# Performance work log

Hardware: AMD Instinct MI355X
Metric: run time of the kernel (lower is better)

The kernel has to match this reference:

```python
import jax, jax.numpy as jnp
import numpy as np
from jax import lax

C = 64
KD = 16  # in_channels // k_factor
KS = 3
DN = ('NCHW', 'OIHW', 'NCHW')


def setup_inputs() -> dict:
    key = jax.random.key(0)
    ks = jax.random.split(key, 9)
    B, H, W = 4, 128, 128
    s = 0.05
    return {
        'x': jax.random.normal(ks[0], (B, C, H, W), jnp.float32),
        'y': jax.random.normal(ks[1], (B, C, H, W), jnp.float32),
        'z': jax.random.normal(ks[2], (B, C, H, W), jnp.float32),
        'Wq': jax.random.normal(ks[3], (C, 1, KS, KS), jnp.float32) * s,   # depthwise
        'bq': jax.random.normal(ks[4], (C,), jnp.float32) * s,
        'Wk': jax.random.normal(ks[5], (KD, C, KS, KS), jnp.float32) * s,
        'bk': jax.random.normal(ks[6], (KD,), jnp.float32) * s,
        'wv': jax.random.normal(ks[7], (KD,), jnp.float32) * s,           # 1x1 conv 1->KD
        'bv': jax.random.normal(ks[8], (KD,), jnp.float32) * s,
    }


def reference(x, y, z, Wq, bq, Wk, bk, wv, bv):
    # Q: depthwise 3x3 conv + ReLU on y -> [B,C,H,W]
    q = jax.nn.relu(
        lax.conv_general_dilated(y, Wq, (1, 1), 'SAME',
                                 dimension_numbers=DN, feature_group_count=C)
        + bq[None, :, None, None])
    # K: 3x3 conv C->KD + ReLU on x -> [B,KD,H,W], shared across the C channel axis
    k = jax.nn.relu(
        lax.conv_general_dilated(x, Wk, (1, 1), 'SAME', dimension_numbers=DN)
        + bk[None, :, None, None])
    # V: 1x1 conv 1->KD + ReLU applied per input channel of z -> [B,C,KD,H,W]
    v = jax.nn.relu(z[:, :, None] * wv[None, None, :, None, None]
                    + bv[None, None, :, None, None])
    # Degenerate SDPA: head_dim=1 so scale=1; softmax over the KD 'sequence' axis.
    scores = q[:, :, None] * k[:, None]              # [B,C,KD,H,W]
    attn = jax.nn.softmax(scores, axis=2)
    return jnp.sum(attn * v, axis=2)                 # [B,C,H,W]
```

## Files before the change

kernel.cpp:

```cpp
#include <hip/hip_runtime.h>

#define HH 128
#define WW 128
#define CC 64
#define KD 16
#define HW (HH * WW)
#define HWB (HW * 4)
#define TOTBYTES (4u * CC * HW * 4u)
#define OOB_SENT 0x40000000

typedef __attribute__((ext_vector_type(4))) int   int32x4_t;
typedef __attribute__((ext_vector_type(4))) float floatx4;
typedef __attribute__((ext_vector_type(2))) float floatx2;

__device__ floatx4 llvm_amdgcn_raw_buffer_load_v4f32(int32x4_t srsrc, int voffset,
                                                     int soffset, int aux)
    __asm("llvm.amdgcn.raw.buffer.load.v4f32");
__device__ floatx2 llvm_amdgcn_raw_buffer_load_v2f32(int32x4_t srsrc, int voffset,
                                                     int soffset, int aux)
    __asm("llvm.amdgcn.raw.buffer.load.v2f32");

__device__ inline int32x4_t make_srd(const void* p, unsigned bytes) {
    const unsigned long long a = (unsigned long long)p;
    int32x4_t r;
    r.x = (int)(a & 0xffffffffull);
    r.y = (int)(a >> 32);
    r.z = (int)bytes;
    r.w = 0x00020000;
    return r;
}

#if __has_builtin(__builtin_amdgcn_exp2f)
#define FAST_EXP2(x) __builtin_amdgcn_exp2f(x)
#define KLOG2E 1.44269504088896340736f
#else
#define FAST_EXP2(x) __expf(x)
#define KLOG2E 1.0f
#endif

__global__ __launch_bounds__(512, 4) void gatev_fused(
    const float* __restrict__ x, const float* __restrict__ y,
    const float* __restrict__ z,
    const float* __restrict__ Wq, const float* __restrict__ bq,
    const float* __restrict__ Wk, const float* __restrict__ bk,
    const float* __restrict__ wv, const float* __restrict__ bv,
    float* __restrict__ out)
{
    __shared__ float lds[16384];

    const int tid  = threadIdx.x;
    const int g    = __builtin_amdgcn_readfirstlane(tid >> 6);
    const int lane = tid & 63;
    const int px16 = lane & 15, py = lane >> 4;
    const int b    = blockIdx.z;
    const int w0   = blockIdx.x * 32 + px16 * 2;
    const int h    = blockIdx.y * 4 + py;
    const int pix  = h * WW + w0;
    const int p0   = py * 32 + px16 * 2;

    const int32x4_t rx = make_srd(x, TOTBYTES);
    const int32x4_t ry = make_srd(y, TOTBYTES);
    const int32x4_t rz = make_srd(z, TOTBYTES);

    const int colb = (w0 > 0 ? w0 - 1 : 0) * 4;
    int rowB[3];
#pragma unroll
    for (int r = 0; r < 3; ++r) {
        const int rr = h - 1 + r;
        rowB[r] = (rr >= 0 && rr < HH) ? rr * WW * 4 + colb : OOB_SENT;
    }
    const float mL = (w0 > 0) ? 1.f : 0.f;
    const float mR = (w0 + 2 < WW) ? 1.f : 0.f;
    const bool  w0e = (w0 == 0);

    const int base = b * CC * HWB;
    const int c0   = __builtin_amdgcn_readfirstlane(g * 8);

    {
        const int d  = tid & 15;
        const int cA = tid >> 4;
#pragma unroll
        for (int half = 0; half < 2; ++half) {
            const int c   = cA + half * 32;
            const int dst = (c >> 3) * 1152 + (c & 7) * 144 + d;
            const float* src = Wk + (d * CC + c) * 9;
#pragma unroll
            for (int t = 0; t < 9; ++t)
                lds[dst + t * 16] = src[t];
        }
    }
    __syncthreads();

    floatx2 aP0[8], aP1[8];
#pragma unroll
    for (int i = 0; i < 8; ++i) { aP0[i] = (floatx2){0.f, 0.f}; aP1[i] = (floatx2){0.f, 0.f}; }

    auto load3 = [&](floatx4 (&f)[3], int so) {
#pragma unroll
        for (int r = 0; r < 3; ++r)
            f[r] = llvm_amdgcn_raw_buffer_load_v4f32(rx, rowB[r], so, 0);
    };
    auto mktaps = [&](const floatx4& f, float (&s)[4]) {
        s[0] = f.x * mL;
        s[1] = w0e ? f.x : f.y;
        s[2] = w0e ? f.y : f.z;
        s[3] = (w0e ? f.z : f.w) * mR;
    };
    auto compute = [&](const floatx4 (&f)[3], int wb) {
        float s[3][4];
#pragma unroll
        for (int r = 0; r < 3; ++r) mktaps(f[r], s[r]);
#pragma unroll
        for (int t = 0; t < 9; ++t) {
            const int tr = t / 3, tc = t % 3;
            const floatx2 t0 = {s[tr][tc],     s[tr][tc]};
            const floatx2 t1 = {s[tr][tc + 1], s[tr][tc + 1]};
#pragma unroll
            for (int j = 0; j < 4; ++j) {
                const floatx4 w4 = *(const floatx4*)&lds[wb + t * 16 + j * 4];
                const floatx2 lo = __builtin_shufflevector(w4, w4, 0, 1);
                const floatx2 hi = __builtin_shufflevector(w4, w4, 2, 3);
                aP0[2 * j + 0] = __builtin_elementwise_fma(lo, t0, aP0[2 * j + 0]);
                aP0[2 * j + 1] = __builtin_elementwise_fma(hi, t0, aP0[2 * j + 1]);
                aP1[2 * j + 0] = __builtin_elementwise_fma(lo, t1, aP1[2 * j + 0]);
                aP1[2 * j + 1] = __builtin_elementwise_fma(hi, t1, aP1[2 * j + 1]);
            }
        }
    };

    const int wbase = g * 1152;
    floatx4 f0[3], f1[3];
    load3(f0, base + c0 * HWB);
#pragma unroll
    for (int cp = 0; cp < 4; ++cp) {
        load3(f1, base + (c0 + 2 * cp + 1) * HWB);
        compute(f0, wbase + (2 * cp) * 144);
        load3(f0, base + (c0 + 2 * cp + 2) * HWB);
        compute(f1, wbase + (2 * cp + 1) * 144);
    }
    __syncthreads();

#pragma unroll
    for (int i = 0; i < 8; ++i) {
        *(floatx2*)&lds[g * 2048 + (2 * i + 0) * 128 + p0] = (floatx2){aP0[i].x, aP1[i].x};
        *(floatx2*)&lds[g * 2048 + (2 * i + 1) * 128 + p0] = (floatx2){aP0[i].y, aP1[i].y};
    }
    __syncthreads();

#pragma unroll
    for (int rep = 0; rep < 4; ++rep) {
        const int idx = tid + rep * 512;
        float s = lds[idx];
#pragma unroll
        for (int gg = 1; gg < 8; ++gg) s += lds[gg * 2048 + idx];
        const int d = idx >> 7;
        lds[idx] = fmaxf(s + bk[d], 0.f) * KLOG2E;
    }
    __syncthreads();

    floatx2 kl2[16];
#pragma unroll
    for (int d = 0; d < KD; ++d)
        kl2[d] = *(const floatx2*)&lds[d * 128 + p0];

    auto process = [&](const floatx4 (&f)[3], floatx2 z2, int c) {
        const float* wq = Wq + c * 9;
        float s[3][4];
#pragma unroll
        for (int r = 0; r < 3; ++r) mktaps(f[r], s[r]);
        floatx2 q2 = {bq[c], bq[c]};
#pragma unroll
        for (int t = 0; t < 9; ++t) {
            const int tr = t / 3, tc = t % 3;
            const floatx2 tp2 = {s[tr][tc], s[tr][tc + 1]};
            const floatx2 wq2 = {wq[t], wq[t]};
            q2 = __builtin_elementwise_fma(wq2, tp2, q2);
        }
        const floatx2 zero2 = {0.f, 0.f};
        q2 = __builtin_elementwise_max(q2, zero2);

        floatx2 num2 = zero2, den2 = zero2;
#pragma unroll
        for (int d = 0; d < KD; ++d) {
            const floatx2 s2 = q2 * kl2[d];
            floatx2 e2;
            e2.x = FAST_EXP2(s2.x);
            e2.y = FAST_EXP2(s2.y);
            const floatx2 wv2 = {wv[d], wv[d]};
            const floatx2 bv2 = {bv[d], bv[d]};
            const floatx2 v2 = __builtin_elementwise_max(
                __builtin_elementwise_fma(z2, wv2, bv2), zero2);
            num2 = __builtin_elementwise_fma(e2, v2, num2);
            den2 = den2 + e2;
        }
        floatx2 o2;
        o2.x = __fdividef(num2.x, den2.x);
        o2.y = __fdividef(num2.y, den2.y);
        *(floatx2*)&out[(size_t)b * CC * HW + (size_t)c * HW + pix] = o2;
    };

    floatx4 fy0[3], fy1[3];
    floatx2 z0, z1;
    auto load3y = [&](floatx4 (&f)[3], floatx2& zz, int so) {
#pragma unroll
        for (int r = 0; r < 3; ++r)
            f[r] = llvm_amdgcn_raw_buffer_load_v4f32(ry, rowB[r], so, 0);
        zz = llvm_amdgcn_raw_buffer_load_v2f32(rz, pix * 4, so, 0);
    };

    load3y(fy0, z0, base + c0 * HWB);
#pragma unroll
    for (int cp = 0; cp < 4; ++cp) {
        load3y(fy1, z1, base + (c0 + 2 * cp + 1) * HWB);
        process(fy0, z0, c0 + 2 * cp);
        load3y(fy0, z0, base + (c0 + 2 * cp + 2) * HWB);
        process(fy1, z1, c0 + 2 * cp + 1);
    }
}

extern "C" void kernel_launch(void* const* d_in, const int* in_sizes, int n_in,
                              void* d_out, int out_size, void* d_ws, size_t ws_size,
                              hipStream_t stream) {
    const float* x  = (const float*)d_in[0];
    const float* y  = (const float*)d_in[1];
    const float* z  = (const float*)d_in[2];
    const float* Wq = (const float*)d_in[3];
    const float* bq = (const float*)d_in[4];
    const float* Wk = (const float*)d_in[5];
    const float* bk = (const float*)d_in[6];
    const float* wv = (const float*)d_in[7];
    const float* bv = (const float*)d_in[8];
    float* out = (float*)d_out;

    dim3 grid(WW / 32, HH / 4, 4);
    dim3 block(512);
    hipLaunchKernelGGL(gatev_fused, grid, block, 0, stream,
                       x, y, z, Wq, bq, Wk, bk, wv, bv, out);
}
```

Measured before the change: 43.45 us.

## Compute K conv with fp16 MFMA over LDS-staged, swizzled input tile

Replaces the per-thread FP32 FMA 3x3 conv (C->KD) and its cross-wave LDS reduction with an implicit-GEMM using 16x16x32 f16 MFMA. The x halo tile (6 rows x 34 cols x 64 channels) and Wk are converted to fp16 and staged in XOR-swizzled LDS to avoid bank conflicts. This removes the 8-way partial-sum reduction and most scalar FMA work, but lowers K precision to fp16 inputs and grows LDS use to about 52 KB per block, which may reduce occupancy.

Result: slower. 115.9 us (+166.8%).

```diff
diff --git a/kernel.cpp b/kernel.cpp
--- a/kernel.cpp
+++ b/kernel.cpp
@@ -12,6 +12,7 @@
 typedef __attribute__((ext_vector_type(4))) int   int32x4_t;
 typedef __attribute__((ext_vector_type(4))) float floatx4;
 typedef __attribute__((ext_vector_type(2))) float floatx2;
+typedef _Float16 f16x8 __attribute__((ext_vector_type(8)));
 
 __device__ floatx4 llvm_amdgcn_raw_buffer_load_v4f32(int32x4_t srsrc, int voffset,
                                                      int soffset, int aux)
@@ -19,6 +20,9 @@
 __device__ floatx2 llvm_amdgcn_raw_buffer_load_v2f32(int32x4_t srsrc, int voffset,
                                                      int soffset, int aux)
     __asm("llvm.amdgcn.raw.buffer.load.v2f32");
+__device__ float llvm_amdgcn_raw_buffer_load_f32(int32x4_t srsrc, int voffset,
+                                                 int soffset, int aux)
+    __asm("llvm.amdgcn.raw.buffer.load.f32");
 
 __device__ inline int32x4_t make_srd(const void* p, unsigned bytes) {
     const unsigned long long a = (unsigned long long)p;
@@ -46,15 +50,20 @@
     const float* __restrict__ wv, const float* __restrict__ bv,
     float* __restrict__ out)
 {
-    __shared__ float lds[16384];
+    __shared__ __align__(16) unsigned char smem[52736];
+    unsigned short* xt   = (unsigned short*)smem;
+    unsigned short* wkl  = (unsigned short*)(smem + 26112);
+    float*          klds = (float*)(smem + 44544);
 
     const int tid  = threadIdx.x;
     const int g    = __builtin_amdgcn_readfirstlane(tid >> 6);
     const int lane = tid & 63;
     const int px16 = lane & 15, py = lane >> 4;
     const int b    = blockIdx.z;
-    const int w0   = blockIdx.x * 32 + px16 * 2;
-    const int h    = blockIdx.y * 4 + py;
+    const int h0   = blockIdx.y * 4;
+    const int w0b  = blockIdx.x * 32;
+    const int w0   = w0b + px16 * 2;
+    const int h    = h0 + py;
     const int pix  = h * WW + w0;
     const int p0   = py * 32 + px16 * 2;
 
@@ -62,6 +71,101 @@
     const int32x4_t ry = make_srd(y, TOTBYTES);
     const int32x4_t rz = make_srd(z, TOTBYTES);
 
+    const int base = b * CC * HWB;
+    const int c0   = __builtin_amdgcn_readfirstlane(g * 8);
+
+    {
+        const int c  = tid & 63;
+        const int jj = tid >> 6;
+        const int so = base + c * HWB;
+#pragma unroll
+        for (int r6 = 0; r6 < 6; ++r6) {
+            const int ir    = h0 - 1 + r6;
+            const bool rok  = (unsigned)ir < (unsigned)HH;
+#pragma unroll
+            for (int s = 0; s < 2; ++s) {
+                const int cp  = jj + 8 * s;
+                const int col = 1 + 2 * cp;
+                const int ic0 = w0b + 2 * cp;
+                const int voff = rok ? (ir * WW + ic0) * 4 : OOB_SENT;
+                const floatx2 v = llvm_amdgcn_raw_buffer_load_v2f32(rx, voff, so, 0);
+                const int pos0 = r6 * 34 + col;
+                const unsigned short h0v = __builtin_bit_cast(unsigned short, (_Float16)v.x);
+                const unsigned short h1v = __builtin_bit_cast(unsigned short, (_Float16)v.y);
+                xt[pos0 * 64       + (((c >> 3) ^ (col & 7)) << 3)       + (c & 7)] = h0v;
+                xt[(pos0 + 1) * 64 + (((c >> 3) ^ ((col + 1) & 7)) << 3) + (c & 7)] = h1v;
+            }
+        }
+        if (tid < 384) {
+            const int cc = tid & 63;
+            const int r6 = tid >> 6;
+            const int ir = h0 - 1 + r6;
+            const bool rok = (unsigned)ir < (unsigned)HH;
+            const int soc = base + cc * HWB;
+            {
+                const int ic = w0b - 1;
+                const int voff = (rok && ic >= 0) ? (ir * WW + ic) * 4 : OOB_SENT;
+                const float v = llvm_amdgcn_raw_buffer_load_f32(rx, voff, soc, 0);
+                xt[(r6 * 34 + 0) * 64 + ((cc >> 3) << 3) + (cc & 7)] =
+                    __builtin_bit_cast(unsigned short, (_Float16)v);
+            }
+            {
+                const int ic = w0b + 32;
+                const int voff = (rok && ic < WW) ? (ir * WW + ic) * 4 : OOB_SENT;
+                const float v = llvm_amdgcn_raw_buffer_load_f32(rx, voff, soc, 0);
+                xt[(r6 * 34 + 33) * 64 + (((cc >> 3) ^ 1) << 3) + (cc & 7)] =
+                    __builtin_bit_cast(unsigned short, (_Float16)v);
+            }
+        }
+    }
+
+#pragma unroll
+    for (int rep = 0; rep < 9; ++rep) {
+        const int idx2 = tid + rep * 512;
+        const int e0   = idx2 * 2;
+        const int c    = e0 & 63;
+        const int d    = (e0 >> 6) & 15;
+        const int t    = e0 >> 10;
+        const float a  = Wk[(d * CC + c) * 9 + t];
+        const float b2 = Wk[(d * CC + c + 1) * 9 + t];
+        const unsigned short ua = __builtin_bit_cast(unsigned short, (_Float16)a);
+        const unsigned short ub = __builtin_bit_cast(unsigned short, (_Float16)b2);
+        const int gsw  = ((c >> 3) ^ (d & 7));
+        const int addr = (t * 16 + d) * 64 + gsw * 8 + (c & 7);
+        *(unsigned*)(wkl + addr) = (unsigned)ua | ((unsigned)ub << 16);
+    }
+    __syncthreads();
+
+    {
+        const int gy = g >> 1;
+        const int gx = g & 1;
+        const int m  = lane & 15;
+        const int q  = lane >> 4;
+
+        floatx4 acc = {0.f, 0.f, 0.f, 0.f};
+#pragma unroll
+        for (int cv = 0; cv < 2; ++cv) {
+#pragma unroll
+            for (int t = 0; t < 9; ++t) {
+                const int trow = t / 3, tcol = t % 3;
+                const int ga = (cv * 4 + q) ^ (m & 7);
+                const f16x8 af = *(const f16x8*)(wkl + ((t * 16 + m) * 64 + ga * 8));
+                const int col = gx * 16 + m + tcol;
+                const int pos = (gy + trow) * 34 + col;
+                const int gb  = (cv * 4 + q) ^ (col & 7);
+                const f16x8 bf = *(const f16x8*)(xt + (pos * 64 + gb * 8));
+                acc = __builtin_amdgcn_mfma_f32_16x16x32_f16(af, bf, acc, 0, 0, 0);
+            }
+        }
+        const int p = gy * 32 + gx * 16 + m;
+#pragma unroll
+        for (int i = 0; i < 4; ++i) {
+            const int d = q * 4 + i;
+            klds[d * 128 + p] = fmaxf(acc[i] + bk[d], 0.f) * KLOG2E;
+        }
+    }
+    __syncthreads();
+
     const int colb = (w0 > 0 ? w0 - 1 : 0) * 4;
     int rowB[3];
 #pragma unroll
@@ -73,95 +177,17 @@
     const float mR = (w0 + 2 < WW) ? 1.f : 0.f;
     const bool  w0e = (w0 == 0);
 
-    const int base = b * CC * HWB;
-    const int c0   = __builtin_amdgcn_readfirstlane(g * 8);
-
-    {
-        const int d  = tid & 15;
-        const int cA = tid >> 4;
-#pragma unroll
-        for (int half = 0; half < 2; ++half) {
-            const int c   = cA + half * 32;
-            const int dst = (c >> 3) * 1152 + (c & 7) * 144 + d;
-            const float* src = Wk + (d * CC + c) * 9;
-#pragma unroll
-            for (int t = 0; t < 9; ++t)
-                lds[dst + t * 16] = src[t];
-        }
-    }
-    __syncthreads();
-
-    floatx2 aP0[8], aP1[8];
-#pragma unroll
-    for (int i = 0; i < 8; ++i) { aP0[i] = (floatx2){0.f, 0.f}; aP1[i] = (floatx2){0.f, 0.f}; }
-
-    auto load3 = [&](floatx4 (&f)[3], int so) {
-#pragma unroll
-        for (int r = 0; r < 3; ++r)
-            f[r] = llvm_amdgcn_raw_buffer_load_v4f32(rx, rowB[r], so, 0);
-    };
+    floatx2 kl2[16];
+#pragma unroll
+    for (int d = 0; d < KD; ++d)
+        kl2[d] = *(const floatx2*)&klds[d * 128 + p0];
+
     auto mktaps = [&](const floatx4& f, float (&s)[4]) {
         s[0] = f.x * mL;
         s[1] = w0e ? f.x : f.y;
         s[2] = w0e ? f.y : f.z;
         s[3] = (w0e ? f.z : f.w) * mR;
     };
-    auto compute = [&](const floatx4 (&f)[3], int wb) {
-        float s[3][4];
-#pragma unroll
-        for (int r = 0; r < 3; ++r) mktaps(f[r], s[r]);
-#pragma unroll
-        for (int t = 0; t < 9; ++t) {
-            const int tr = t / 3, tc = t % 3;
-            const floatx2 t0 = {s[tr][tc],     s[tr][tc]};
-            const floatx2 t1 = {s[tr][tc + 1], s[tr][tc + 1]};
-#pragma unroll
-            for (int j = 0; j < 4; ++j) {
-                const floatx4 w4 = *(const floatx4*)&lds[wb + t * 16 + j * 4];
-                const floatx2 lo = __builtin_shufflevector(w4, w4, 0, 1);
-                const floatx2 hi = __builtin_shufflevector(w4, w4, 2, 3);
-                aP0[2 * j + 0] = __builtin_elementwise_fma(lo, t0, aP0[2 * j + 0]);
-                aP0[2 * j + 1] = __builtin_elementwise_fma(hi, t0, aP0[2 * j + 1]);
-                aP1[2 * j + 0] = __builtin_elementwise_fma(lo, t1, aP1[2 * j + 0]);
-                aP1[2 * j + 1] = __builtin_elementwise_fma(hi, t1, aP1[2 * j + 1]);
-            }
-        }
-    };
-
-    const int wbase = g * 1152;
-    floatx4 f0[3], f1[3];
-    load3(f0, base + c0 * HWB);
-#pragma unroll
-    for (int cp = 0; cp < 4; ++cp) {
-        load3(f1, base + (c0 + 2 * cp + 1) * HWB);
-        compute(f0, wbase + (2 * cp) * 144);
-        load3(f0, base + (c0 + 2 * cp + 2) * HWB);
-        compute(f1, wbase + (2 * cp + 1) * 144);
-    }
-    __syncthreads();
-
-#pragma unroll
-    for (int i = 0; i < 8; ++i) {
-        *(floatx2*)&lds[g * 2048 + (2 * i + 0) * 128 + p0] = (floatx2){aP0[i].x, aP1[i].x};
-        *(floatx2*)&lds[g * 2048 + (2 * i + 1) * 128 + p0] = (floatx2){aP0[i].y, aP1[i].y};
-    }
-    __syncthreads();
-
-#pragma unroll
-    for (int rep = 0; rep < 4; ++rep) {
-        const int idx = tid + rep * 512;
-        float s = lds[idx];
-#pragma unroll
-        for (int gg = 1; gg < 8; ++gg) s += lds[gg * 2048 + idx];
-        const int d = idx >> 7;
-        lds[idx] = fmaxf(s + bk[d], 0.f) * KLOG2E;
-    }
-    __syncthreads();
-
-    floatx2 kl2[16];
-#pragma unroll
-    for (int d = 0; d < KD; ++d)
-        kl2[d] = *(const floatx2*)&lds[d * 128 + p0];
 
     auto process = [&](const floatx4 (&f)[3], floatx2 z2, int c) {
         const float* wq = Wq + c * 9;
```

## Repack Wk in a pre-kernel and read conv weights from global instead of LDS

Applied to the files above, without the earlier changes.

Adds a small repack kernel that lays Wk out into workspace in the [c][tap][d] order the main kernel consumes. The main kernel now reads weights straight from global memory (wave-uniform, likely scalar or cached loads) instead of staging them in LDS. This drops the per-block strided LDS fill and one barrier. It also adds a fast path that skips the edge masking for blocks away from the image's left and right borders, at the cost of an extra kernel launch and global weight loads inside the inner loop.

Result: slower. 48.98 us (+12.7%).

```diff
diff --git a/kernel.cpp b/kernel.cpp
--- a/kernel.cpp
+++ b/kernel.cpp
@@ -38,11 +38,22 @@
 #define KLOG2E 1.0f
 #endif
 
+__global__ __launch_bounds__(512, 1) void repack_wk(const float* __restrict__ Wk,
+                                                    float* __restrict__ wsr) {
+    const int e = blockIdx.x * 512 + threadIdx.x;
+    const int d = e & 15;
+    const int r = e >> 4;
+    const int t = r % 9;
+    const int c = r / 9;
+    wsr[e] = Wk[(d * CC + c) * 9 + t];
+}
+
 __global__ __launch_bounds__(512, 4) void gatev_fused(
     const float* __restrict__ x, const float* __restrict__ y,
     const float* __restrict__ z,
+    const float* __restrict__ wsr,
     const float* __restrict__ Wq, const float* __restrict__ bq,
-    const float* __restrict__ Wk, const float* __restrict__ bk,
+    const float* __restrict__ bk,
     const float* __restrict__ wv, const float* __restrict__ bv,
     float* __restrict__ out)
 {
@@ -69,6 +80,7 @@
         const int rr = h - 1 + r;
         rowB[r] = (rr >= 0 && rr < HH) ? rr * WW * 4 + colb : OOB_SENT;
     }
+    const bool  intw = (blockIdx.x > 0) & (blockIdx.x < (WW / 32 - 1));
     const float mL = (w0 > 0) ? 1.f : 0.f;
     const float mR = (w0 + 2 < WW) ? 1.f : 0.f;
     const bool  w0e = (w0 == 0);
@@ -76,20 +88,15 @@
     const int base = b * CC * HWB;
     const int c0   = __builtin_amdgcn_readfirstlane(g * 8);
 
-    {
-        const int d  = tid & 15;
-        const int cA = tid >> 4;
-#pragma unroll
-        for (int half = 0; half < 2; ++half) {
-            const int c   = cA + half * 32;
-            const int dst = (c >> 3) * 1152 + (c & 7) * 144 + d;
-            const float* src = Wk + (d * CC + c) * 9;
-#pragma unroll
-            for (int t = 0; t < 9; ++t)
-                lds[dst + t * 16] = src[t];
-        }
-    }
-    __syncthreads();
+    auto mktaps = [&](const floatx4& f, float (&s)[4]) {
+        if (intw) { s[0] = f.x; s[1] = f.y; s[2] = f.z; s[3] = f.w; }
+        else {
+            s[0] = f.x * mL;
+            s[1] = w0e ? f.x : f.y;
+            s[2] = w0e ? f.y : f.z;
+            s[3] = (w0e ? f.z : f.w) * mR;
+        }
+    };
 
     floatx2 aP0[8], aP1[8];
 #pragma unroll
@@ -100,13 +107,7 @@
         for (int r = 0; r < 3; ++r)
             f[r] = llvm_amdgcn_raw_buffer_load_v4f32(rx, rowB[r], so, 0);
     };
-    auto mktaps = [&](const floatx4& f, float (&s)[4]) {
-        s[0] = f.x * mL;
-        s[1] = w0e ? f.x : f.y;
-        s[2] = w0e ? f.y : f.z;
-        s[3] = (w0e ? f.z : f.w) * mR;
-    };
-    auto compute = [&](const floatx4 (&f)[3], int wb) {
+    auto compute = [&](const floatx4 (&f)[3], const float* wp) {
         float s[3][4];
 #pragma unroll
         for (int r = 0; r < 3; ++r) mktaps(f[r], s[r]);
@@ -117,7 +118,7 @@
             const floatx2 t1 = {s[tr][tc + 1], s[tr][tc + 1]};
 #pragma unroll
             for (int j = 0; j < 4; ++j) {
-                const floatx4 w4 = *(const floatx4*)&lds[wb + t * 16 + j * 4];
+                const floatx4 w4 = *(const floatx4*)&wp[t * 16 + j * 4];
                 const floatx2 lo = __builtin_shufflevector(w4, w4, 0, 1);
                 const floatx2 hi = __builtin_shufflevector(w4, w4, 2, 3);
                 aP0[2 * j + 0] = __builtin_elementwise_fma(lo, t0, aP0[2 * j + 0]);
@@ -128,17 +129,17 @@
         }
     };
 
-    const int wbase = g * 1152;
-    floatx4 f0[3], f1[3];
-    load3(f0, base + c0 * HWB);
-#pragma unroll
-    for (int cp = 0; cp < 4; ++cp) {
-        load3(f1, base + (c0 + 2 * cp + 1) * HWB);
-        compute(f0, wbase + (2 * cp) * 144);
-        load3(f0, base + (c0 + 2 * cp + 2) * HWB);
-        compute(f1, wbase + (2 * cp + 1) * 144);
-    }
-    __syncthreads();
+    {
+        floatx4 f0[3], f1[3];
+        load3(f0, base + c0 * HWB);
+#pragma unroll
+        for (int cp = 0; cp < 4; ++cp) {
+            load3(f1, base + (c0 + 2 * cp + 1) * HWB);
+            compute(f0, wsr + (c0 + 2 * cp) * 144);
+            load3(f0, base + (c0 + 2 * cp + 2) * HWB);
+            compute(f1, wsr + (c0 + 2 * cp + 1) * 144);
+        }
+    }
 
 #pragma unroll
     for (int i = 0; i < 8; ++i) {
@@ -199,8 +200,6 @@
         *(floatx2*)&out[(size_t)b * CC * HW + (size_t)c * HW + pix] = o2;
     };
 
-    floatx4 fy0[3], fy1[3];
-    floatx2 z0, z1;
     auto load3y = [&](floatx4 (&f)[3], floatx2& zz, int so) {
 #pragma unroll
         for (int r = 0; r < 3; ++r)
@@ -208,13 +207,17 @@
         zz = llvm_amdgcn_raw_buffer_load_v2f32(rz, pix * 4, so, 0);
     };
 
-    load3y(fy0, z0, base + c0 * HWB);
-#pragma unroll
-    for (int cp = 0; cp < 4; ++cp) {
-        load3y(fy1, z1, base + (c0 + 2 * cp + 1) * HWB);
-        process(fy0, z0, c0 + 2 * cp);
-        load3y(fy0, z0, base + (c0 + 2 * cp + 2) * HWB);
-        process(fy1, z1, c0 + 2 * cp + 1);
+    {
+        floatx4 fy0[3], fy1[3];
+        floatx2 z0, z1;
+        load3y(fy0, z0, base + c0 * HWB);
+#pragma unroll
+        for (int cp = 0; cp < 4; ++cp) {
+            load3y(fy1, z1, base + (c0 + 2 * cp + 1) * HWB);
+            process(fy0, z0, c0 + 2 * cp);
+            load3y(fy0, z0, base + (c0 + 2 * cp + 2) * HWB);
+            process(fy1, z1, c0 + 2 * cp + 1);
+        }
     }
 }
 
@@ -231,9 +234,12 @@
     const float* wv = (const float*)d_in[7];
     const float* bv = (const float*)d_in[8];
     float* out = (float*)d_out;
+    float* wsr = (float*)d_ws;
+
+    hipLaunchKernelGGL(repack_wk, dim3(18), dim3(512), 0, stream, Wk, wsr);
 
     dim3 grid(WW / 32, HH / 4, 4);
     dim3 block(512);
     hipLaunchKernelGGL(gatev_fused, grid, block, 0, stream,
-                       x, y, z, Wq, bq, Wk, bk, wv, bv, out);
-}
+                       x, y, z, wsr, Wq, bq, bk, wv, bv, out);
+}
```
